# Kernel tuning notes

Hardware: AMD Instinct MI355X
Metric: run time of the kernel (lower is better)

Reference implementation:

```python
import jax, jax.numpy as jnp
import numpy as np

B, S, D, H, K, MLP, ZD = 8, 2048, 1024, 16, 256, 4096, 1024
DH = D // H
EPS = 1e-6


def setup_inputs() -> dict:
    key = jax.random.key(0)
    ks = jax.random.split(key, 32)
    g = lambda i, shape, scale=0.02: jax.random.normal(ks[i], shape, dtype=jnp.float32) * scale
    inp = {
        "x": jax.random.normal(ks[0], (B, S, D), dtype=jnp.float32),
        "z": jax.random.normal(ks[1], (B, ZD), dtype=jnp.float32),
        # attention projections
        "wq": g(2, (D, D)), "bq": jnp.zeros((D,), jnp.float32),
        "wk": g(3, (D, D)), "bk": jnp.zeros((D,), jnp.float32),
        "wv": g(4, (D, D)), "bv": jnp.zeros((D,), jnp.float32),
        # Linformer sequence projections (kernel over seq dim)
        "Ew": g(5, (S, K)), "Eb": jnp.zeros((K,), jnp.float32),
        "Fw": g(6, (S, K)), "Fb": jnp.zeros((K,), jnp.float32),
        "wo": g(7, (D, D)), "bo": jnp.zeros((D,), jnp.float32),
        # adaLN 1
        "h1w": g(8, (ZD, D)), "h1b": jnp.zeros((D,), jnp.float32),
        "g1w": g(9, (D, D)), "g1b": jnp.ones((D,), jnp.float32),
        "be1w": g(10, (D, D)), "be1b": jnp.zeros((D,), jnp.float32),
        # adaLN 2
        "h2w": g(11, (ZD, D)), "h2b": jnp.zeros((D,), jnp.float32),
        "g2w": g(12, (D, D)), "g2b": jnp.ones((D,), jnp.float32),
        "be2w": g(13, (D, D)), "be2b": jnp.zeros((D,), jnp.float32),
        # MLP
        "m1w": g(14, (D, MLP)), "m1b": jnp.zeros((MLP,), jnp.float32),
        "m2w": g(15, (MLP, D)), "m2b": jnp.zeros((D,), jnp.float32),
    }
    return inp


def _adaln(x, z, hw, hb, gw, gb, bw, bb):
    # moments over feature axis, normalize, then conditioned scale/shift
    mean = jnp.mean(x, axis=2, keepdims=True)
    var = jnp.var(x, axis=2, keepdims=True)
    xn = (x - mean) * jax.lax.rsqrt(var + EPS)
    h = jax.nn.silu(z @ hw + hb)              # [B, D]
    scale = h @ gw + gb                        # [B, D]
    offset = h @ bw + bb                       # [B, D]
    return xn * scale[:, None, :] + offset[:, None, :]


def _linformer_attn(x, wq, bq, wk, bk, wv, bv, Ew, Eb, Fw, Fb, wo, bo):
    q = (x @ wq + bq).reshape(B, S, H, DH).transpose(0, 2, 1, 3)  # [B,H,S,dh]
    k = (x @ wk + bk).reshape(B, S, H, DH).transpose(0, 2, 1, 3)
    v = (x @ wv + bv).reshape(B, S, H, DH).transpose(0, 2, 1, 3)
    # project seq dim S -> K (Dense applied to [B,H,dh,S]); bias adds on K axis
    k = jnp.einsum('bhsd,sk->bhkd', k, Ew) + Eb[None, None, :, None]  # [B,H,K,dh]
    v = jnp.einsum('bhsd,sk->bhkd', v, Fw) + Fb[None, None, :, None]
    scores = jnp.einsum('bhsd,bhkd->bhsk', q, k) / jnp.sqrt(jnp.float32(DH))
    attn = jax.nn.softmax(scores, axis=-1)
    out = jnp.einsum('bhsk,bhkd->bhsd', attn, v)  # [B,H,S,dh]
    out = out.transpose(0, 2, 1, 3).reshape(B, S, D)
    return out @ wo + bo


def reference(x, z, wq, bq, wk, bk, wv, bv, Ew, Eb, Fw, Fb, wo, bo,
              h1w, h1b, g1w, g1b, be1w, be1b,
              h2w, h2b, g2w, g2b, be2w, be2b,
              m1w, m1b, m2w, m2b):
    x1 = _adaln(x, z, h1w, h1b, g1w, g1b, be1w, be1b)
    attn_out = x + _linformer_attn(x1, wq, bq, wk, bk, wv, bv, Ew, Eb, Fw, Fb, wo, bo)
    x2 = _adaln(attn_out, z, h2w, h2b, g2w, g2b, be2w, be2b)
    hmid = jax.nn.gelu(x2 @ m1w + m1b, approximate=False)
    mlp_out = hmid @ m2w + m2b
    return mlp_out + attn_out
```

## Files before the change

### kernel.cpp

```cpp
#include <hip/hip_runtime.h>
#include <math.h>

#define AS1 __attribute__((address_space(1)))
#define AS3 __attribute__((address_space(3)))

typedef short bf16x8 __attribute__((ext_vector_type(8)));
typedef short s16x4  __attribute__((ext_vector_type(4)));
typedef float f32x4  __attribute__((ext_vector_type(4)));

#define MFMA(a,b,c) __builtin_amdgcn_mfma_f32_16x16x32_bf16((a),(b),(c),0,0,0)

__device__ __forceinline__ short f2bf(float f) {
  union { float f; unsigned u; } v; v.f = f;
  unsigned r = v.u + 0x7FFFu + ((v.u >> 16) & 1u);
  return (short)(r >> 16);
}

__device__ __forceinline__ void gload16(const void* g, void* l) {
  __builtin_amdgcn_global_load_lds((const AS1 void*)g, (AS3 void*)l, 16, 0, 0);
}

__global__ __launch_bounds__(256) void k_transpose_cvt(
    const float* __restrict__ in, short* __restrict__ out, int R, int C) {
  __shared__ float t[64][65];
  int c0 = blockIdx.x * 64, r0 = blockIdx.y * 64;
  int tx = threadIdx.x & 63, ty = threadIdx.x >> 6;
  for (int r = ty; r < 64; r += 4)
    t[r][tx] = in[(size_t)(r0 + r) * C + c0 + tx];
  __syncthreads();
  for (int c = ty; c < 64; c += 4)
    out[(size_t)(c0 + c) * R + r0 + tx] = f2bf(t[tx][c]);
}

__global__ __launch_bounds__(256) void k_cond_h(
    const float* __restrict__ z,
    const float* __restrict__ h1w, const float* __restrict__ h1b,
    const float* __restrict__ h2w, const float* __restrict__ h2b,
    float* __restrict__ hbuf) {
  int dl = threadIdx.x & 63, kq = threadIdx.x >> 6;
  int d = blockIdx.x * 64 + dl;
  int b = blockIdx.y, sel = blockIdx.z;
  const float* W = (sel ? h2w : h1w) + (size_t)(kq * 256) * 1024 + d;
  const float* zr = z + b * 1024 + kq * 256;
  float acc = 0.f;
  for (int i = 0; i < 256; ++i) acc = fmaf(zr[i], W[(size_t)i * 1024], acc);
  __shared__ float red[256];
  red[threadIdx.x] = acc;
  __syncthreads();
  if (kq == 0) {
    float v = red[dl] + red[dl + 64] + red[dl + 128] + red[dl + 192];
    v += (sel ? h2b : h1b)[d];
    hbuf[(size_t)(sel * 8 + b) * 1024 + d] = v / (1.f + expf(-v));
  }
}

__global__ __launch_bounds__(256) void k_cond_so(
    const float* __restrict__ hbuf,
    const float* __restrict__ g1w, const float* __restrict__ g1b,
    const float* __restrict__ be1w, const float* __restrict__ be1b,
    const float* __restrict__ g2w, const float* __restrict__ g2b,
    const float* __restrict__ be2w, const float* __restrict__ be2b,
    float* __restrict__ so) {
  int dl = threadIdx.x & 63, kq = threadIdx.x >> 6;
  int d = blockIdx.x * 64 + dl;
  int b = blockIdx.y, sel = blockIdx.z;
  const float* W = sel == 0 ? g1w : sel == 1 ? be1w : sel == 2 ? g2w : be2w;
  const float* bias = sel == 0 ? g1b : sel == 1 ? be1b : sel == 2 ? g2b : be2b;
  const float* hr = hbuf + (size_t)((sel >> 1) * 8 + b) * 1024 + kq * 256;
  const float* Wp = W + (size_t)(kq * 256) * 1024 + d;
  float acc = 0.f;
  for (int i = 0; i < 256; ++i) acc = fmaf(hr[i], Wp[(size_t)i * 1024], acc);
  __shared__ float red[256];
  red[threadIdx.x] = acc;
  __syncthreads();
  if (kq == 0) {
    float v = red[dl] + red[dl + 64] + red[dl + 128] + red[dl + 192] + bias[d];
    so[(size_t)(sel * 8 + b) * 1024 + d] = v;
  }
}

__global__ __launch_bounds__(256) void k_adaln(
    const float* __restrict__ xin, const float* __restrict__ so,
    int which, short* __restrict__ xout) {
  int row = blockIdx.x;
  int b = row >> 11;
  const float4* xr = (const float4*)(xin + (size_t)row * 1024);
  float4 v = xr[threadIdx.x];
  float s = v.x + v.y + v.z + v.w;
  float sq = v.x * v.x + v.y * v.y + v.z * v.z + v.w * v.w;
#pragma unroll
  for (int o = 32; o >= 1; o >>= 1) {
    s += __shfl_xor(s, o, 64);
    sq += __shfl_xor(sq, o, 64);
  }
  __shared__ float red[8];
  int wid = threadIdx.x >> 6;
  if ((threadIdx.x & 63) == 0) { red[wid] = s; red[4 + wid] = sq; }
  __syncthreads();
  s = red[0] + red[1] + red[2] + red[3];
  sq = red[4] + red[5] + red[6] + red[7];
  float mean = s * (1.f / 1024.f);
  float var = sq * (1.f / 1024.f) - mean * mean;
  float rstd = rsqrtf(var + 1e-6f);
  const float4* scp = (const float4*)(so + (size_t)(which * 2) * 8192 + b * 1024);
  const float4* ofp = (const float4*)(so + (size_t)(which * 2 + 1) * 8192 + b * 1024);
  float4 sc = scp[threadIdx.x], of = ofp[threadIdx.x];
  s16x4 o;
  o[0] = f2bf((v.x - mean) * rstd * sc.x + of.x);
  o[1] = f2bf((v.y - mean) * rstd * sc.y + of.y);
  o[2] = f2bf((v.z - mean) * rstd * sc.z + of.z);
  o[3] = f2bf((v.w - mean) * rstd * sc.w + of.w);
  *(s16x4*)(xout + (size_t)row * 1024 + threadIdx.x * 4) = o;
}

enum { EPI_QKV = 0, EPI_KP = 1, EPI_VPT = 2, EPI_RESID = 3, EPI_GELU = 4 };

template <int EPI>
__global__ __launch_bounds__(256) void k_gemm(
    const short* __restrict__ A, long sA, int lda,
    const short* __restrict__ BT, long sBT, int ldbt,
    int Kd,
    short* __restrict__ o0, short* __restrict__ o1, short* __restrict__ o2,
    const float* __restrict__ b0, const float* __restrict__ b1,
    const float* __restrict__ b2,
    const float* __restrict__ resid, float* __restrict__ fo, long sC) {
  int t = threadIdx.x, lane = t & 63, wid = t >> 6;
  int wr = wid >> 1, wc = wid & 1;
  int n0 = blockIdx.x * 128, m0 = blockIdx.y * 128, bz = blockIdx.z;
  const short* Ab = A + (long)bz * sA;
  const short* Bb = BT + (long)bz * sBT;
  __shared__ short lds[8192];
  const short* gA = Ab + (long)(m0 + (t >> 2)) * lda + (t & 3) * 8;
  const short* gB = Bb + (long)(n0 + (t >> 2)) * ldbt + (t & 3) * 8;
  char* lA = (char*)lds + wid * 1024;
  char* lB = (char*)lds + 8192 + wid * 1024;
  const long a64 = (long)64 * lda, b64s = (long)64 * ldbt;
  f32x4 acc[4][4];
#pragma unroll
  for (int m = 0; m < 4; ++m)
#pragma unroll
    for (int n = 0; n < 4; ++n) acc[m][n] = (f32x4){0.f, 0.f, 0.f, 0.f};

  int rsel = lane & 15, koff = (lane >> 4) * 16;
  for (int k = 0; k < Kd; k += 32) {
    gload16(gA, lA);
    gload16(gA + a64, lA + 4096);
    gload16(gB, lB);
    gload16(gB + b64s, lB + 4096);
    gA += 32; gB += 32;
    __syncthreads();
    bf16x8 af[4], bfr[4];
#pragma unroll
    for (int m = 0; m < 4; ++m)
      af[m] = *(const bf16x8*)((const char*)lds + (wr * 64 + m * 16 + rsel) * 64 + koff);
#pragma unroll
    for (int n = 0; n < 4; ++n)
      bfr[n] = *(const bf16x8*)((const char*)lds + 8192 + (wc * 64 + n * 16 + rsel) * 64 + koff);
#pragma unroll
    for (int m = 0; m < 4; ++m)
#pragma unroll
      for (int n = 0; n < 4; ++n)
        acc[m][n] = MFMA(af[m], bfr[n], acc[m][n]);
    __syncthreads();
  }

  int cl = lane & 15, rh = lane >> 4;
#pragma unroll
  for (int m = 0; m < 4; ++m) {
    int rgb = m0 + wr * 64 + m * 16 + rh * 4;
#pragma unroll
    for (int n = 0; n < 4; ++n) {
      int cg = n0 + wc * 64 + n * 16 + cl;
      f32x4 a = acc[m][n];
      if constexpr (EPI == EPI_QKV) {
        int sec = n0 >> 10;
        int cloc = cg & 1023;
        float bias = (sec == 0 ? b0 : sec == 1 ? b1 : b2)[cloc];
        if (sec == 0) {
#pragma unroll
          for (int r = 0; r < 4; ++r)
            o0[(size_t)(rgb + r) * 1024 + cloc] = f2bf(a[r] + bias);
        } else {
          short* dst = (sec == 1) ? o1 : o2;
          int bb = rgb >> 11, sl = rgb & 2047;
          s16x4 pk;
#pragma unroll
          for (int r = 0; r < 4; ++r) pk[r] = f2bf(a[r] + bias);
          *(s16x4*)(dst + ((long)bb * 1024 + cloc) * 2048 + sl) = pk;
        }
      } else if constexpr (EPI == EPI_KP) {
        short* dst = o0 + (long)bz * sC;
#pragma unroll
        for (int r = 0; r < 4; ++r)
          dst[(size_t)(rgb + r) * 1024 + cg] = f2bf(a[r] + b0[rgb + r]);
      } else if constexpr (EPI == EPI_VPT) {
        short* dst = o0 + (long)bz * sC;
        s16x4 pk;
#pragma unroll
        for (int r = 0; r < 4; ++r) pk[r] = f2bf(a[r] + b0[rgb + r]);
        *(s16x4*)(dst + (long)cg * 256 + rgb) = pk;
      } else if constexpr (EPI == EPI_RESID) {
        float bias = b0[cg];
#pragma unroll
        for (int r = 0; r < 4; ++r) {
          size_t idx = (size_t)(rgb + r) * 1024 + cg;
          fo[idx] = a[r] + bias + resid[idx];
        }
      } else if constexpr (EPI == EPI_GELU) {
        float bias = b0[cg];
#pragma unroll
        for (int r = 0; r < 4; ++r) {
          float xv = a[r] + bias;
          float g = 0.5f * xv * (1.f + erff(xv * 0.70710678118654752f));
          o0[(size_t)(rgb + r) * 4096 + cg] = f2bf(g);
        }
      }
    }
  }
}

__global__ __launch_bounds__(256) void k_attn(
    const short* __restrict__ q, const short* __restrict__ kp,
    const short* __restrict__ vpt, short* __restrict__ oh) {
  int lane = threadIdx.x & 63, wid = threadIdx.x >> 6;
  int h = blockIdx.y, b = blockIdx.z;
  int s0 = blockIdx.x * 64 + wid * 16;
  int cl = lane & 15, rh = lane >> 4;
  __shared__ short plds[4][16][264];

  const short* qbase = q + ((size_t)(b * 2048 + s0 + cl)) * 1024 + h * 64 + rh * 8;
  bf16x8 qa0 = *(const bf16x8*)qbase;
  bf16x8 qa1 = *(const bf16x8*)(qbase + 32);

  f32x4 sc[16];
  const short* kb = kp + ((size_t)(b * 256 + cl)) * 1024 + h * 64 + rh * 8;
#pragma unroll
  for (int n = 0; n < 16; ++n) {
    const short* kn = kb + (size_t)(n * 16) * 1024;
    f32x4 a = (f32x4){0.f, 0.f, 0.f, 0.f};
    a = MFMA(qa0, *(const bf16x8*)kn, a);
    a = MFMA(qa1, *(const bf16x8*)(kn + 32), a);
    sc[n] = a * 0.125f;
  }

  float mx[4] = {-1e30f, -1e30f, -1e30f, -1e30f};
#pragma unroll
  for (int n = 0; n < 16; ++n)
#pragma unroll
    for (int r = 0; r < 4; ++r) mx[r] = fmaxf(mx[r], sc[n][r]);
#pragma unroll
  for (int o = 1; o < 16; o <<= 1)
#pragma unroll
    for (int r = 0; r < 4; ++r) mx[r] = fmaxf(mx[r], __shfl_xor(mx[r], o, 64));

  float sm[4] = {0.f, 0.f, 0.f, 0.f};
#pragma unroll
  for (int n = 0; n < 16; ++n)
#pragma unroll
    for (int r = 0; r < 4; ++r) {
      float e = expf(sc[n][r] - mx[r]);
      sc[n][r] = e;
      sm[r] += e;
    }
#pragma unroll
  for (int o = 1; o < 16; o <<= 1)
#pragma unroll
    for (int r = 0; r < 4; ++r) sm[r] += __shfl_xor(sm[r], o, 64);
  float inv[4];
#pragma unroll
  for (int r = 0; r < 4; ++r) inv[r] = 1.f / sm[r];

#pragma unroll
  for (int n = 0; n < 16; ++n)
#pragma unroll
    for (int r = 0; r < 4; ++r)
      plds[wid][rh * 4 + r][n * 16 + cl] = f2bf(sc[n][r] * inv[r]);
  asm volatile("s_waitcnt lgkmcnt(0)" ::: "memory");

  bf16x8 pa[8];
#pragma unroll
  for (int c = 0; c < 8; ++c)
    pa[c] = *(const bf16x8*)&plds[wid][cl][c * 32 + rh * 8];

  const short* vb = vpt + ((size_t)(b * 1024 + h * 64 + cl)) * 256 + rh * 8;
  short* ob = oh + ((size_t)(b * 2048 + s0 + rh * 4)) * 1024 + h * 64 + cl;
#pragma unroll
  for (int n = 0; n < 4; ++n) {
    f32x4 a = (f32x4){0.f, 0.f, 0.f, 0.f};
    const short* vn = vb + (size_t)(n * 16) * 256;
#pragma unroll
    for (int c = 0; c < 8; ++c)
      a = MFMA(pa[c], *(const bf16x8*)(vn + c * 32), a);
#pragma unroll
    for (int r = 0; r < 4; ++r)
      ob[(size_t)r * 1024 + n * 16] = f2bf(a[r]);
  }
}

extern "C" void kernel_launch(void* const* d_in, const int* in_sizes, int n_in,
                              void* d_out, int out_size, void* d_ws, size_t ws_size,
                              hipStream_t stream) {
  (void)in_sizes; (void)n_in; (void)out_size; (void)ws_size;
  const float* x    = (const float*)d_in[0];
  const float* z    = (const float*)d_in[1];
  const float* wq   = (const float*)d_in[2];
  const float* bq   = (const float*)d_in[3];
  const float* wk   = (const float*)d_in[4];
  const float* bk   = (const float*)d_in[5];
  const float* wv   = (const float*)d_in[6];
  const float* bv   = (const float*)d_in[7];
  const float* Ew   = (const float*)d_in[8];
  const float* Eb   = (const float*)d_in[9];
  const float* Fw   = (const float*)d_in[10];
  const float* Fb   = (const float*)d_in[11];
  const float* wo   = (const float*)d_in[12];
  const float* bo   = (const float*)d_in[13];
  const float* h1w  = (const float*)d_in[14];
  const float* h1b  = (const float*)d_in[15];
  const float* g1w  = (const float*)d_in[16];
  const float* g1b  = (const float*)d_in[17];
  const float* be1w = (const float*)d_in[18];
  const float* be1b = (const float*)d_in[19];
  const float* h2w  = (const float*)d_in[20];
  const float* h2b  = (const float*)d_in[21];
  const float* g2w  = (const float*)d_in[22];
  const float* g2b  = (const float*)d_in[23];
  const float* be2w = (const float*)d_in[24];
  const float* be2b = (const float*)d_in[25];
  const float* m1w  = (const float*)d_in[26];
  const float* m1b  = (const float*)d_in[27];
  const float* m2w  = (const float*)d_in[28];
  const float* m2b  = (const float*)d_in[29];
  float* out = (float*)d_out;

  char* ws = (char*)d_ws;
  size_t off = 0;
  auto alloc = [&](size_t bytes) {
    char* p = ws + off;
    off += (bytes + 255) & ~(size_t)255;
    return p;
  };
  short* x1  = (short*)alloc((size_t)32 << 20);
  short* qb  = (short*)alloc((size_t)32 << 20);
  short* kT  = (short*)alloc((size_t)32 << 20);
  short* vT  = (short*)alloc((size_t)32 << 20);
  short* ah  = (short*)alloc((size_t)32 << 20);
  short* kpj = (short*)alloc((size_t)4 << 20);
  short* vpt = (short*)alloc((size_t)4 << 20);
  short* wqkvT = (short*)alloc((size_t)3072 * 1024 * 2);
  short* woT   = (short*)alloc((size_t)1024 * 1024 * 2);
  short* m1T   = (short*)alloc((size_t)4096 * 1024 * 2);
  short* m2T   = (short*)alloc((size_t)1024 * 4096 * 2);
  short* EwT   = (short*)alloc((size_t)256 * 2048 * 2);
  short* FwT   = (short*)alloc((size_t)256 * 2048 * 2);
  float* hbuf  = (float*)alloc((size_t)2 * 8 * 1024 * 4);
  float* sobuf = (float*)alloc((size_t)4 * 8 * 1024 * 4);
  float* aout = (float*)kT;
  short* x2   = ah;
  short* hmid = x1;

  dim3 blk(256);
  k_transpose_cvt<<<dim3(16, 16), blk, 0, stream>>>(wq, wqkvT, 1024, 1024);
  k_transpose_cvt<<<dim3(16, 16), blk, 0, stream>>>(wk, wqkvT + 1024 * 1024, 1024, 1024);
  k_transpose_cvt<<<dim3(16, 16), blk, 0, stream>>>(wv, wqkvT + 2 * 1024 * 1024, 1024, 1024);
  k_transpose_cvt<<<dim3(16, 16), blk, 0, stream>>>(wo, woT, 1024, 1024);
  k_transpose_cvt<<<dim3(64, 16), blk, 0, stream>>>(m1w, m1T, 1024, 4096);
  k_transpose_cvt<<<dim3(16, 64), blk, 0, stream>>>(m2w, m2T, 4096, 1024);
  k_transpose_cvt<<<dim3(4, 32), blk, 0, stream>>>(Ew, EwT, 2048, 256);
  k_transpose_cvt<<<dim3(4, 32), blk, 0, stream>>>(Fw, FwT, 2048, 256);
  k_cond_h<<<dim3(16, 8, 2), blk, 0, stream>>>(z, h1w, h1b, h2w, h2b, hbuf);
  k_cond_so<<<dim3(16, 8, 4), blk, 0, stream>>>(hbuf, g1w, g1b, be1w, be1b,
                                                g2w, g2b, be2w, be2b, sobuf);
  k_adaln<<<dim3(16384), blk, 0, stream>>>(x, sobuf, 0, x1);
  k_gemm<EPI_QKV><<<dim3(24, 128, 1), blk, 0, stream>>>(
      x1, 0, 1024, wqkvT, 0, 1024, 1024,
      qb, kT, vT, bq, bk, bv, nullptr, nullptr, 0);
  k_gemm<EPI_KP><<<dim3(8, 2, 8), blk, 0, stream>>>(
      EwT, 0, 2048, kT, (long)1024 * 2048, 2048, 2048,
      kpj, nullptr, nullptr, Eb, nullptr, nullptr, nullptr, nullptr, 262144);
  k_gemm<EPI_VPT><<<dim3(8, 2, 8), blk, 0, stream>>>(
      FwT, 0, 2048, vT, (long)1024 * 2048, 2048, 2048,
      vpt, nullptr, nullptr, Fb, nullptr, nullptr, nullptr, nullptr, 262144);
  k_attn<<<dim3(32, 16, 8), blk, 0, stream>>>(qb, kpj, vpt, ah);
  k_gemm<EPI_RESID><<<dim3(8, 128, 1), blk, 0, stream>>>(
      ah, 0, 1024, woT, 0, 1024, 1024,
      nullptr, nullptr, nullptr, bo, nullptr, nullptr, x, aout, 0);
  k_adaln<<<dim3(16384), blk, 0, stream>>>(aout, sobuf, 1, x2);
  for (int c = 0; c < 2; ++c) {
    const short* x2c = x2 + (size_t)c * 8192 * 1024;
    const float* aoc = aout + (size_t)c * 8192 * 1024;
    float* outc = out + (size_t)c * 8192 * 1024;
    k_gemm<EPI_GELU><<<dim3(32, 64, 1), blk, 0, stream>>>(
        x2c, 0, 1024, m1T, 0, 1024, 1024,
        hmid, nullptr, nullptr, m1b, nullptr, nullptr, nullptr, nullptr, 0);
    k_gemm<EPI_RESID><<<dim3(8, 64, 1), blk, 0, stream>>>(
        hmid, 0, 4096, m2T, 0, 4096, 4096,
        nullptr, nullptr, nullptr, m2b, nullptr, nullptr, aoc, outc, 0);
  }
}
```

Before: 1.065 ms.

## Add 256x256-tile 8-wave GEMM with double-buffered LDS pipeline for dense projections

Adds a new GEMM kernel with 256x256 output tiles, 512 threads and a 128 KB double-buffered LDS ring. Global-to-LDS loads are interleaved with phased MFMA blocks, using XOR-swizzled LDS addressing, s_setprio and a grid swizzle for L2 locality. The QKV, output-projection and both MLP GEMMs move to this kernel, while the small Linformer projections keep the old 128-tile kernel. The aim is more data reuse per tile and better overlap of loads with MFMA. The cost is higher register and LDS pressure, and fewer workgroups for the smaller GEMMs (128 and 256 blocks), which may underfill the GPU.

After: 1.116 ms. +4.8%, slower.

```diff
diff --git a/kernel.cpp b/kernel.cpp
--- a/kernel.cpp
+++ b/kernel.cpp
@@ -172,23 +172,7 @@
     for (int n = 0; n < 4; ++n) {
       int cg = n0 + wc * 64 + n * 16 + cl;
       f32x4 a = acc[m][n];
-      if constexpr (EPI == EPI_QKV) {
-        int sec = n0 >> 10;
-        int cloc = cg & 1023;
-        float bias = (sec == 0 ? b0 : sec == 1 ? b1 : b2)[cloc];
-        if (sec == 0) {
-#pragma unroll
-          for (int r = 0; r < 4; ++r)
-            o0[(size_t)(rgb + r) * 1024 + cloc] = f2bf(a[r] + bias);
-        } else {
-          short* dst = (sec == 1) ? o1 : o2;
-          int bb = rgb >> 11, sl = rgb & 2047;
-          s16x4 pk;
-#pragma unroll
-          for (int r = 0; r < 4; ++r) pk[r] = f2bf(a[r] + bias);
-          *(s16x4*)(dst + ((long)bb * 1024 + cloc) * 2048 + sl) = pk;
-        }
-      } else if constexpr (EPI == EPI_KP) {
+      if constexpr (EPI == EPI_KP) {
         short* dst = o0 + (long)bz * sC;
 #pragma unroll
         for (int r = 0; r < 4; ++r)
@@ -199,15 +183,155 @@
 #pragma unroll
         for (int r = 0; r < 4; ++r) pk[r] = f2bf(a[r] + b0[rgb + r]);
         *(s16x4*)(dst + (long)cg * 256 + rgb) = pk;
+      }
+    }
+  }
+}
+
+template <int EPI>
+__global__ __launch_bounds__(512, 2) void k_gemm256(
+    const short* __restrict__ A, int lda,
+    const short* __restrict__ BT, int ldbt,
+    int Kd, int ntN,
+    short* __restrict__ o0, short* __restrict__ o1, short* __restrict__ o2,
+    const float* __restrict__ bi0, const float* __restrict__ bi1,
+    const float* __restrict__ bi2,
+    const float* __restrict__ resid, float* __restrict__ fo) {
+  __shared__ __align__(16) char lds[131072];
+  int t = threadIdx.x, lane = t & 63, wid = t >> 6;
+  int wr = wid >> 2, wc = wid & 3;
+  int l15 = lane & 15;
+  int lko = ((lane >> 4) * 16) ^ (((l15 >> 2) & 1) << 5);
+
+  int nwg = gridDim.x, o = blockIdx.x;
+  int swz = (o & 7) * (nwg >> 3) + (o >> 3);
+  int mt = swz / ntN, nt = swz - mt * ntN;
+  int m0 = mt * 256, n0 = nt * 256;
+
+  int p0 = t * 16;
+  int sl = p0 ^ (((p0 >> 9) & 1) << 5);
+  int srow = sl >> 7, scol = sl & 127;
+  const char* A8 = (const char*)A;
+  const char* B8 = (const char*)BT;
+  size_t ldab = (size_t)lda * 2, ldbb = (size_t)ldbt * 2;
+  size_t aoff = (size_t)(m0 + srow) * ldab + scol;
+  size_t boff = (size_t)(n0 + srow) * ldbb + scol;
+  char* ldsw = (char*)lds + wid * 1024;
+
+  auto stage = [&](int H, int kt, int buf) {
+    char* d = ldsw + buf * 65536 + H * 16384;
+    if (H < 2) {
+      const char* s = A8 + aoff + (size_t)(H * 128) * ldab + (size_t)kt * 128;
+      gload16(s, d);
+      gload16(s + 64 * ldab, d + 8192);
+    } else {
+      const char* s = B8 + boff + (size_t)((H - 2) * 128) * ldbb + (size_t)kt * 128;
+      gload16(s, d);
+      gload16(s + 64 * ldbb, d + 8192);
+    }
+  };
+
+  const char* LA = (const char*)lds + wr * 16384 + l15 * 128 + lko;
+  const char* LB = (const char*)lds + 32768 + (wc >> 1) * 16384 + (wc & 1) * 8192 +
+                   l15 * 128 + lko;
+
+  f32x4 acc[8][4];
+#pragma unroll
+  for (int m = 0; m < 8; ++m)
+#pragma unroll
+    for (int n = 0; n < 4; ++n) acc[m][n] = (f32x4){0.f, 0.f, 0.f, 0.f};
+
+  bf16x8 af[4][2], Bv0[2][2], Bv1[2][2];
+
+#define RDA(buf, mi, ks) (*(const bf16x8*)(LA + (buf) * 65536 + (mi) * 2048 + (ks) * 64))
+#define RDB(buf, ni, ks) (*(const bf16x8*)(LB + (buf) * 65536 + (ni) * 2048 + (ks) * 64))
+#define PH_TAIL(MB, NB, BARR)                                         \
+  __builtin_amdgcn_s_barrier();                                       \
+  asm volatile("s_waitcnt lgkmcnt(0)" ::: "memory");                  \
+  __builtin_amdgcn_sched_barrier(0);                                  \
+  __builtin_amdgcn_s_setprio(1);                                      \
+  _Pragma("unroll") for (int mi = 0; mi < 4; ++mi)                    \
+  _Pragma("unroll") for (int ni = 0; ni < 2; ++ni)                    \
+  _Pragma("unroll") for (int ks = 0; ks < 2; ++ks)                    \
+      acc[(MB) + mi][(NB) + ni] =                                     \
+          MFMA(af[mi][ks], BARR[ni][ks], acc[(MB) + mi][(NB) + ni]);  \
+  __builtin_amdgcn_s_setprio(0);                                      \
+  __builtin_amdgcn_s_barrier();
+
+  int NT = Kd >> 6, NI = NT >> 1, msk = NT - 1;
+
+  stage(0, 0, 0); stage(1, 0, 0); stage(2, 0, 0); stage(3, 0, 0);
+  stage(0, 1, 1);
+  asm volatile("s_waitcnt vmcnt(2)" ::: "memory");
+  __builtin_amdgcn_s_barrier();
+
+  auto half = [&](int bf, int tkA, int bufA, int tkB, int bufB) {
+#pragma unroll
+    for (int mi = 0; mi < 4; ++mi)
+#pragma unroll
+      for (int ks = 0; ks < 2; ++ks) af[mi][ks] = RDA(bf, mi, ks);
+#pragma unroll
+    for (int ni = 0; ni < 2; ++ni)
+#pragma unroll
+      for (int ks = 0; ks < 2; ++ks) Bv0[ni][ks] = RDB(bf, ni, ks);
+    stage(1, tkA, bufA);
+    PH_TAIL(0, 0, Bv0)
+#pragma unroll
+    for (int ni = 0; ni < 2; ++ni)
+#pragma unroll
+      for (int ks = 0; ks < 2; ++ks) Bv1[ni][ks] = RDB(bf, ni + 2, ks);
+    stage(2, tkA, bufA);
+    PH_TAIL(0, 2, Bv1)
+#pragma unroll
+    for (int mi = 0; mi < 4; ++mi)
+#pragma unroll
+      for (int ks = 0; ks < 2; ++ks) af[mi][ks] = RDA(bf, mi + 4, ks);
+    stage(3, tkA, bufA);
+    PH_TAIL(4, 2, Bv1)
+    stage(0, tkB, bufB);
+    asm volatile("s_waitcnt vmcnt(2)" ::: "memory");
+    PH_TAIL(4, 0, Bv0)
+  };
+
+  for (int i = 0; i < NI; ++i) {
+    int T1k = 2 * i + 1, T2k = (2 * i + 2) & msk, T3k = (2 * i + 3) & msk;
+    half(0, T1k, 1, T2k, 0);
+    half(1, T2k, 0, T3k, 1);
+  }
+
+  int cl = l15, rh = lane >> 4;
+#pragma unroll
+  for (int m = 0; m < 8; ++m) {
+    int rgb = m0 + wr * 128 + m * 16 + rh * 4;
+#pragma unroll
+    for (int n = 0; n < 4; ++n) {
+      int cg = n0 + wc * 64 + n * 16 + cl;
+      f32x4 a = acc[m][n];
+      if constexpr (EPI == EPI_QKV) {
+        int sec = n0 >> 10;
+        int cloc = cg & 1023;
+        float bias = (sec == 0 ? bi0 : sec == 1 ? bi1 : bi2)[cloc];
+        if (sec == 0) {
+#pragma unroll
+          for (int r = 0; r < 4; ++r)
+            o0[(size_t)(rgb + r) * 1024 + cloc] = f2bf(a[r] + bias);
+        } else {
+          short* dst = (sec == 1) ? o1 : o2;
+          int bb = rgb >> 11, slc = rgb & 2047;
+          s16x4 pk;
+#pragma unroll
+          for (int r = 0; r < 4; ++r) pk[r] = f2bf(a[r] + bias);
+          *(s16x4*)(dst + ((long)bb * 1024 + cloc) * 2048 + slc) = pk;
+        }
       } else if constexpr (EPI == EPI_RESID) {
-        float bias = b0[cg];
+        float bias = bi0[cg];
 #pragma unroll
         for (int r = 0; r < 4; ++r) {
           size_t idx = (size_t)(rgb + r) * 1024 + cg;
           fo[idx] = a[r] + bias + resid[idx];
         }
       } else if constexpr (EPI == EPI_GELU) {
-        float bias = b0[cg];
+        float bias = bi0[cg];
 #pragma unroll
         for (int r = 0; r < 4; ++r) {
           float xv = a[r] + bias;
@@ -217,6 +341,9 @@
       }
     }
   }
+#undef RDA
+#undef RDB
+#undef PH_TAIL
 }
 
 __global__ __launch_bounds__(256) void k_attn(
@@ -372,9 +499,9 @@
   k_cond_so<<<dim3(16, 8, 4), blk, 0, stream>>>(hbuf, g1w, g1b, be1w, be1b,
                                                 g2w, g2b, be2w, be2b, sobuf);
   k_adaln<<<dim3(16384), blk, 0, stream>>>(x, sobuf, 0, x1);
-  k_gemm<EPI_QKV><<<dim3(24, 128, 1), blk, 0, stream>>>(
-      x1, 0, 1024, wqkvT, 0, 1024, 1024,
-      qb, kT, vT, bq, bk, bv, nullptr, nullptr, 0);
+  k_gemm256<EPI_QKV><<<dim3(768), dim3(512), 0, stream>>>(
+      x1, 1024, wqkvT, 1024, 1024, 12,
+      qb, kT, vT, bq, bk, bv, nullptr, nullptr);
   k_gemm<EPI_KP><<<dim3(8, 2, 8), blk, 0, stream>>>(
       EwT, 0, 2048, kT, (long)1024 * 2048, 2048, 2048,
       kpj, nullptr, nullptr, Eb, nullptr, nullptr, nullptr, nullptr, 262144);
@@ -382,19 +509,19 @@
       FwT, 0, 2048, vT, (long)1024 * 2048, 2048, 2048,
       vpt, nullptr, nullptr, Fb, nullptr, nullptr, nullptr, nullptr, 262144);
   k_attn<<<dim3(32, 16, 8), blk, 0, stream>>>(qb, kpj, vpt, ah);
-  k_gemm<EPI_RESID><<<dim3(8, 128, 1), blk, 0, stream>>>(
-      ah, 0, 1024, woT, 0, 1024, 1024,
-      nullptr, nullptr, nullptr, bo, nullptr, nullptr, x, aout, 0);
+  k_gemm256<EPI_RESID><<<dim3(256), dim3(512), 0, stream>>>(
+      ah, 1024, woT, 1024, 1024, 4,
+      nullptr, nullptr, nullptr, bo, nullptr, nullptr, x, aout);
   k_adaln<<<dim3(16384), blk, 0, stream>>>(aout, sobuf, 1, x2);
   for (int c = 0; c < 2; ++c) {
     const short* x2c = x2 + (size_t)c * 8192 * 1024;
     const float* aoc = aout + (size_t)c * 8192 * 1024;
     float* outc = out + (size_t)c * 8192 * 1024;
-    k_gemm<EPI_GELU><<<dim3(32, 64, 1), blk, 0, stream>>>(
-        x2c, 0, 1024, m1T, 0, 1024, 1024,
-        hmid, nullptr, nullptr, m1b, nullptr, nullptr, nullptr, nullptr, 0);
-    k_gemm<EPI_RESID><<<dim3(8, 64, 1), blk, 0, stream>>>(
-        hmid, 0, 4096, m2T, 0, 4096, 4096,
-        nullptr, nullptr, nullptr, m2b, nullptr, nullptr, aoc, outc, 0);
-  }
-}
+    k_gemm256<EPI_GELU><<<dim3(512), dim3(512), 0, stream>>>(
+        x2c, 1024, m1T, 1024, 1024, 16,
+        hmid, nullptr, nullptr, m1b, nullptr, nullptr, nullptr, nullptr);
+    k_gemm256<EPI_RESID><<<dim3(128), dim3(512), 0, stream>>>(
+        hmid, 4096, m2T, 4096, 4096, 4,
+        nullptr, nullptr, nullptr, m2b, nullptr, nullptr, aoc, outc);
+  }
+}
```

## Merge K/V Linformer projections into one launch and add 256x256 GEMM for MLP1

Applied to the files above, without the earlier changes.

Combines the separate K and V sequence-projection GEMMs into a single launch, using the z grid dimension to select which one a block computes. Adds a new 512-thread GEMM kernel with 256x256 tiles, double-buffered LDS with swizzled layout, grid swizzle and MFMA priority bumps, and uses it for the first MLP up-projection chunk. The aim is to cut launch overhead and improve data reuse and latency hiding in the largest GEMM. In exchange it uses 128KB of LDS per block, which limits occupancy, and the second chunk still runs on the old kernel.

After: 1.167 ms. 1.1x slower.

```diff
diff --git a/kernel.cpp b/kernel.cpp
--- a/kernel.cpp
+++ b/kernel.cpp
@@ -113,7 +113,7 @@
   *(s16x4*)(xout + (size_t)row * 1024 + threadIdx.x * 4) = o;
 }
 
-enum { EPI_QKV = 0, EPI_KP = 1, EPI_VPT = 2, EPI_RESID = 3, EPI_GELU = 4 };
+enum { EPI_QKV = 0, EPI_KVP = 1, EPI_RESID = 3, EPI_GELU = 4 };
 
 template <int EPI>
 __global__ __launch_bounds__(256) void k_gemm(
@@ -127,8 +127,17 @@
   int t = threadIdx.x, lane = t & 63, wid = t >> 6;
   int wr = wid >> 1, wc = wid & 1;
   int n0 = blockIdx.x * 128, m0 = blockIdx.y * 128, bz = blockIdx.z;
-  const short* Ab = A + (long)bz * sA;
-  const short* Bb = BT + (long)bz * sBT;
+  int batch = bz, sel = 0;
+  if constexpr (EPI == EPI_KVP) { batch = bz & 7; sel = bz >> 3; }
+  const short* Ab;
+  const short* Bb;
+  if constexpr (EPI == EPI_KVP) {
+    Ab = sel ? (const short*)o2 : A;
+    Bb = BT + (long)sel * 16777216 + (long)batch * sBT;
+  } else {
+    Ab = A + (long)batch * sA;
+    Bb = BT + (long)batch * sBT;
+  }
   __shared__ short lds[8192];
   const short* gA = Ab + (long)(m0 + (t >> 2)) * lda + (t & 3) * 8;
   const short* gB = Bb + (long)(n0 + (t >> 2)) * ldbt + (t & 3) * 8;
@@ -188,17 +197,19 @@
           for (int r = 0; r < 4; ++r) pk[r] = f2bf(a[r] + bias);
           *(s16x4*)(dst + ((long)bb * 1024 + cloc) * 2048 + sl) = pk;
         }
-      } else if constexpr (EPI == EPI_KP) {
-        short* dst = o0 + (long)bz * sC;
-#pragma unroll
-        for (int r = 0; r < 4; ++r)
-          dst[(size_t)(rgb + r) * 1024 + cg] = f2bf(a[r] + b0[rgb + r]);
-      } else if constexpr (EPI == EPI_VPT) {
-        short* dst = o0 + (long)bz * sC;
-        s16x4 pk;
-#pragma unroll
-        for (int r = 0; r < 4; ++r) pk[r] = f2bf(a[r] + b0[rgb + r]);
-        *(s16x4*)(dst + (long)cg * 256 + rgb) = pk;
+      } else if constexpr (EPI == EPI_KVP) {
+        const float* bias = sel ? b1 : b0;
+        short* dst = (sel ? o1 : o0) + (long)batch * sC;
+        if (sel == 0) {
+#pragma unroll
+          for (int r = 0; r < 4; ++r)
+            dst[(size_t)(rgb + r) * 1024 + cg] = f2bf(a[r] + bias[rgb + r]);
+        } else {
+          s16x4 pk;
+#pragma unroll
+          for (int r = 0; r < 4; ++r) pk[r] = f2bf(a[r] + bias[rgb + r]);
+          *(s16x4*)(dst + (long)cg * 256 + rgb) = pk;
+        }
       } else if constexpr (EPI == EPI_RESID) {
         float bias = b0[cg];
 #pragma unroll
@@ -213,6 +224,119 @@
           float xv = a[r] + bias;
           float g = 0.5f * xv * (1.f + erff(xv * 0.70710678118654752f));
           o0[(size_t)(rgb + r) * 4096 + cg] = f2bf(g);
+        }
+      }
+    }
+  }
+}
+
+template <int EPI>
+__global__ __launch_bounds__(512, 2) void k_gemm256p2(
+    const short* __restrict__ A, int lda,
+    const short* __restrict__ BT, int ldbt,
+    int Kd, int ntN,
+    short* __restrict__ o0, const float* __restrict__ bi0,
+    const float* __restrict__ resid, float* __restrict__ fo) {
+  __shared__ __align__(16) char lds[131072];
+  int t = threadIdx.x, lane = t & 63, wid = t >> 6;
+  int wr = wid >> 2, wc = wid & 3;
+  int l15 = lane & 15;
+  int q16x = ((lane >> 4) * 16) ^ ((l15 & 3) << 4);
+  int kf64 = ((l15 >> 2) & 1) << 6;
+  int k0o = kf64, k1o = 64 - kf64;
+
+  int nwg = gridDim.x, o = blockIdx.x;
+  int swz = (o & 7) * (nwg >> 3) + (o >> 3);
+  int mt = swz / ntN, nt = swz - mt * ntN;
+  int m0 = mt * 256, n0 = nt * 256;
+
+  int p0 = t * 16;
+  int srow = p0 >> 7;
+  int scol = (p0 & 127) ^ ((srow & 7) << 4);
+  size_t ldab = (size_t)lda * 2, ldbb = (size_t)ldbt * 2;
+  const char* sA0 = (const char*)A + (size_t)(m0 + srow) * ldab + scol;
+  const char* sA1 = sA0 + 128 * ldab;
+  const char* sB0 = (const char*)BT + (size_t)(n0 + srow) * ldbb + scol;
+  const char* sB1 = sB0 + 128 * ldbb;
+  char* ldsw = (char*)lds + wid * 1024;
+  size_t a64 = ldab << 6, b64 = ldbb << 6;
+
+  auto stage = [&](int kt, int buf) {
+    char* d = ldsw + buf * 65536;
+    size_t ko = (size_t)kt << 7;
+    gload16(sA0 + ko, d);           gload16(sA0 + ko + a64, d + 8192);
+    gload16(sA1 + ko, d + 16384);   gload16(sA1 + ko + a64, d + 24576);
+    gload16(sB0 + ko, d + 32768);   gload16(sB0 + ko + b64, d + 40960);
+    gload16(sB1 + ko, d + 49152);   gload16(sB1 + ko + b64, d + 57344);
+  };
+
+  const char* LAb = (const char*)lds + wr * 16384 + l15 * 128 + q16x;
+  const char* LBb = (const char*)lds + 32768 + (wc >> 1) * 16384 + (wc & 1) * 8192 +
+                    l15 * 128 + q16x;
+
+  f32x4 acc[8][4];
+#pragma unroll
+  for (int m = 0; m < 8; ++m)
+#pragma unroll
+    for (int n = 0; n < 4; ++n) acc[m][n] = (f32x4){0.f, 0.f, 0.f, 0.f};
+
+  int NT = Kd >> 6;
+  stage(0, 0);
+  asm volatile("s_waitcnt vmcnt(0)" ::: "memory");
+  __builtin_amdgcn_s_barrier();
+
+  for (int tt = 0; tt < NT; ++tt) {
+    int cur = tt & 1;
+    int nxt = (tt + 1 < NT) ? tt + 1 : 0;
+    stage(nxt, cur ^ 1);
+    const char* LA = LAb + cur * 65536;
+    const char* LB = LBb + cur * 65536;
+    bf16x8 af[8][2], bfr[4][2];
+#pragma unroll
+    for (int mi = 0; mi < 8; ++mi)
+#pragma unroll
+      for (int ks = 0; ks < 2; ++ks)
+        af[mi][ks] = *(const bf16x8*)(LA + mi * 2048 + (ks ? k1o : k0o));
+#pragma unroll
+    for (int ni = 0; ni < 4; ++ni)
+#pragma unroll
+      for (int ks = 0; ks < 2; ++ks)
+        bfr[ni][ks] = *(const bf16x8*)(LB + ni * 2048 + (ks ? k1o : k0o));
+    __builtin_amdgcn_s_setprio(1);
+#pragma unroll
+    for (int mi = 0; mi < 8; ++mi)
+#pragma unroll
+      for (int ni = 0; ni < 4; ++ni)
+#pragma unroll
+        for (int ks = 0; ks < 2; ++ks)
+          acc[mi][ni] = MFMA(af[mi][ks], bfr[ni][ks], acc[mi][ni]);
+    __builtin_amdgcn_s_setprio(0);
+    asm volatile("s_waitcnt vmcnt(0)" ::: "memory");
+    __builtin_amdgcn_s_barrier();
+  }
+
+  int cl = l15, rh = lane >> 4;
+#pragma unroll
+  for (int m = 0; m < 8; ++m) {
+    int rgb = m0 + wr * 128 + m * 16 + rh * 4;
+#pragma unroll
+    for (int n = 0; n < 4; ++n) {
+      int cg = n0 + wc * 64 + n * 16 + cl;
+      f32x4 a = acc[m][n];
+      if constexpr (EPI == EPI_GELU) {
+        float bias = bi0[cg];
+#pragma unroll
+        for (int r = 0; r < 4; ++r) {
+          float xv = a[r] + bias;
+          float g = 0.5f * xv * (1.f + erff(xv * 0.70710678118654752f));
+          o0[(size_t)(rgb + r) * 4096 + cg] = f2bf(g);
+        }
+      } else if constexpr (EPI == EPI_RESID) {
+        float bias = bi0[cg];
+#pragma unroll
+        for (int r = 0; r < 4; ++r) {
+          size_t idx = (size_t)(rgb + r) * 1024 + cg;
+          fo[idx] = a[r] + bias + resid[idx];
         }
       }
     }
@@ -375,21 +499,23 @@
   k_gemm<EPI_QKV><<<dim3(24, 128, 1), blk, 0, stream>>>(
       x1, 0, 1024, wqkvT, 0, 1024, 1024,
       qb, kT, vT, bq, bk, bv, nullptr, nullptr, 0);
-  k_gemm<EPI_KP><<<dim3(8, 2, 8), blk, 0, stream>>>(
+  k_gemm<EPI_KVP><<<dim3(8, 2, 16), blk, 0, stream>>>(
       EwT, 0, 2048, kT, (long)1024 * 2048, 2048, 2048,
-      kpj, nullptr, nullptr, Eb, nullptr, nullptr, nullptr, nullptr, 262144);
-  k_gemm<EPI_VPT><<<dim3(8, 2, 8), blk, 0, stream>>>(
-      FwT, 0, 2048, vT, (long)1024 * 2048, 2048, 2048,
-      vpt, nullptr, nullptr, Fb, nullptr, nullptr, nullptr, nullptr, 262144);
+      kpj, vpt, FwT, Eb, Fb, nullptr, nullptr, nullptr, 262144);
   k_attn<<<dim3(32, 16, 8), blk, 0, stream>>>(qb, kpj, vpt, ah);
   k_gemm<EPI_RESID><<<dim3(8, 128, 1), blk, 0, stream>>>(
       ah, 0, 1024, woT, 0, 1024, 1024,
       nullptr, nullptr, nullptr, bo, nullptr, nullptr, x, aout, 0);
   k_adaln<<<dim3(16384), blk, 0, stream>>>(aout, sobuf, 1, x2);
-  for (int c = 0; c < 2; ++c) {
-    const short* x2c = x2 + (size_t)c * 8192 * 1024;
-    const float* aoc = aout + (size_t)c * 8192 * 1024;
-    float* outc = out + (size_t)c * 8192 * 1024;
+  k_gemm256p2<EPI_GELU><<<dim3(512), dim3(512), 0, stream>>>(
+      x2, 1024, m1T, 1024, 1024, 16, hmid, m1b, nullptr, nullptr);
+  k_gemm<EPI_RESID><<<dim3(8, 64, 1), blk, 0, stream>>>(
+      hmid, 0, 4096, m2T, 0, 4096, 4096,
+      nullptr, nullptr, nullptr, m2b, nullptr, nullptr, aout, out, 0);
+  {
+    const short* x2c = x2 + (size_t)8192 * 1024;
+    const float* aoc = aout + (size_t)8192 * 1024;
+    float* outc = out + (size_t)8192 * 1024;
     k_gemm<EPI_GELU><<<dim3(32, 64, 1), blk, 0, stream>>>(
         x2c, 0, 1024, m1T, 0, 1024, 1024,
         hmid, nullptr, nullptr, m1b, nullptr, nullptr, nullptr, nullptr, 0);
```

## Reassociate Linformer K/V projections to project x over sequence first

Applied to the files above, without the earlier changes.

Instead of computing full K and V projections over all 2048 positions and then projecting the sequence down to 256, the code first projects the normalized input x1 along the sequence with E and F (via a bf16 transpose of x1). It then applies wk/wv to the reduced 256-row tensors, folding the biases in through column sums of E and F. This removes two large S×D×D GEMMs and their transposed writes, at the cost of an extra transpose pass over x1. The four square weight transposes are also merged into one launch, and the first MLP up-projection chunk uses a new 64-wide-K swizzled GEMM kernel.

Measured after the change: 1.107 ms. +3.9%, slower.

```diff
diff --git a/kernel.cpp b/kernel.cpp
--- a/kernel.cpp
+++ b/kernel.cpp
@@ -30,6 +30,48 @@
   __syncthreads();
   for (int c = ty; c < 64; c += 4)
     out[(size_t)(c0 + c) * R + r0 + tx] = f2bf(t[tx][c]);
+}
+
+__global__ __launch_bounds__(256) void k_transpose_cvt4(
+    const float* __restrict__ s0, const float* __restrict__ s1,
+    const float* __restrict__ s2, const float* __restrict__ s3,
+    short* __restrict__ d0, short* __restrict__ d1,
+    short* __restrict__ d2, short* __restrict__ d3) {
+  int zz = blockIdx.z;
+  const float* in = zz == 0 ? s0 : zz == 1 ? s1 : zz == 2 ? s2 : s3;
+  short* out = zz == 0 ? d0 : zz == 1 ? d1 : zz == 2 ? d2 : d3;
+  __shared__ float t[64][65];
+  int c0 = blockIdx.x * 64, r0 = blockIdx.y * 64;
+  int tx = threadIdx.x & 63, ty = threadIdx.x >> 6;
+  for (int r = ty; r < 64; r += 4)
+    t[r][tx] = in[(size_t)(r0 + r) * 1024 + c0 + tx];
+  __syncthreads();
+  for (int c = ty; c < 64; c += 4)
+    out[(size_t)(c0 + c) * 1024 + r0 + tx] = f2bf(t[tx][c]);
+}
+
+__global__ __launch_bounds__(256) void k_transpose_bf16(
+    const short* __restrict__ in, short* __restrict__ out) {
+  __shared__ short t[64][65];
+  int d0 = blockIdx.x * 64, s0 = blockIdx.y * 64, b = blockIdx.z;
+  int tx = threadIdx.x & 63, ty = threadIdx.x >> 6;
+  const short* src = in + ((size_t)(b * 2048 + s0)) * 1024 + d0;
+  for (int r = ty; r < 64; r += 4)
+    t[r][tx] = src[(size_t)r * 1024 + tx];
+  __syncthreads();
+  short* dst = out + ((size_t)(b * 1024 + d0)) * 2048 + s0;
+  for (int c = ty; c < 64; c += 4)
+    dst[(size_t)c * 2048 + tx] = t[tx][c];
+}
+
+__global__ __launch_bounds__(256) void k_colsum(
+    const float* __restrict__ Ew, const float* __restrict__ Fw,
+    float* __restrict__ cs) {
+  int ki = threadIdx.x, sel = blockIdx.x;
+  const float* W = sel ? Fw : Ew;
+  float s = 0.f;
+  for (int i = 0; i < 2048; ++i) s += W[(size_t)i * 256 + ki];
+  cs[sel * 256 + ki] = s;
 }
 
 __global__ __launch_bounds__(256) void k_cond_h(
@@ -113,7 +155,7 @@
   *(s16x4*)(xout + (size_t)row * 1024 + threadIdx.x * 4) = o;
 }
 
-enum { EPI_QKV = 0, EPI_KP = 1, EPI_VPT = 2, EPI_RESID = 3, EPI_GELU = 4 };
+enum { EPI_Q = 0, EPI_EF = 1, EPI_RESID = 3, EPI_GELU = 4 };
 
 template <int EPI>
 __global__ __launch_bounds__(256) void k_gemm(
@@ -121,14 +163,22 @@
     const short* __restrict__ BT, long sBT, int ldbt,
     int Kd,
     short* __restrict__ o0, short* __restrict__ o1, short* __restrict__ o2,
-    const float* __restrict__ b0, const float* __restrict__ b1,
-    const float* __restrict__ b2,
+    const float* __restrict__ b0,
     const float* __restrict__ resid, float* __restrict__ fo, long sC) {
   int t = threadIdx.x, lane = t & 63, wid = t >> 6;
   int wr = wid >> 1, wc = wid & 1;
   int n0 = blockIdx.x * 128, m0 = blockIdx.y * 128, bz = blockIdx.z;
-  const short* Ab = A + (long)bz * sA;
-  const short* Bb = BT + (long)bz * sBT;
+  int batch = bz, sel = 0;
+  if constexpr (EPI == EPI_EF) { batch = bz & 7; sel = bz >> 3; }
+  const short* Ab;
+  const short* Bb;
+  if constexpr (EPI == EPI_EF) {
+    Ab = sel ? (const short*)o2 : A;
+    Bb = BT + (long)batch * sBT;
+  } else {
+    Ab = A + (long)batch * sA;
+    Bb = BT + (long)batch * sBT;
+  }
   __shared__ short lds[8192];
   const short* gA = Ab + (long)(m0 + (t >> 2)) * lda + (t & 3) * 8;
   const short* gB = Bb + (long)(n0 + (t >> 2)) * ldbt + (t & 3) * 8;
@@ -172,33 +222,16 @@
     for (int n = 0; n < 4; ++n) {
       int cg = n0 + wc * 64 + n * 16 + cl;
       f32x4 a = acc[m][n];
-      if constexpr (EPI == EPI_QKV) {
-        int sec = n0 >> 10;
-        int cloc = cg & 1023;
-        float bias = (sec == 0 ? b0 : sec == 1 ? b1 : b2)[cloc];
-        if (sec == 0) {
-#pragma unroll
-          for (int r = 0; r < 4; ++r)
-            o0[(size_t)(rgb + r) * 1024 + cloc] = f2bf(a[r] + bias);
-        } else {
-          short* dst = (sec == 1) ? o1 : o2;
-          int bb = rgb >> 11, sl = rgb & 2047;
-          s16x4 pk;
-#pragma unroll
-          for (int r = 0; r < 4; ++r) pk[r] = f2bf(a[r] + bias);
-          *(s16x4*)(dst + ((long)bb * 1024 + cloc) * 2048 + sl) = pk;
-        }
-      } else if constexpr (EPI == EPI_KP) {
-        short* dst = o0 + (long)bz * sC;
+      if constexpr (EPI == EPI_Q) {
+        float bias = b0[cg];
 #pragma unroll
         for (int r = 0; r < 4; ++r)
-          dst[(size_t)(rgb + r) * 1024 + cg] = f2bf(a[r] + b0[rgb + r]);
-      } else if constexpr (EPI == EPI_VPT) {
-        short* dst = o0 + (long)bz * sC;
-        s16x4 pk;
-#pragma unroll
-        for (int r = 0; r < 4; ++r) pk[r] = f2bf(a[r] + b0[rgb + r]);
-        *(s16x4*)(dst + (long)cg * 256 + rgb) = pk;
+          o0[(size_t)(rgb + r) * 1024 + cg] = f2bf(a[r] + bias);
+      } else if constexpr (EPI == EPI_EF) {
+        short* dst = (sel ? o1 : o0) + (long)batch * sC;
+#pragma unroll
+        for (int r = 0; r < 4; ++r)
+          dst[(size_t)(rgb + r) * 1024 + cg] = f2bf(a[r]);
       } else if constexpr (EPI == EPI_RESID) {
         float bias = b0[cg];
 #pragma unroll
@@ -214,6 +247,154 @@
           float g = 0.5f * xv * (1.f + erff(xv * 0.70710678118654752f));
           o0[(size_t)(rgb + r) * 4096 + cg] = f2bf(g);
         }
+      }
+    }
+  }
+}
+
+__global__ __launch_bounds__(256) void k_kvproj(
+    const short* __restrict__ xe, const short* __restrict__ xf,
+    const short* __restrict__ wkT, const short* __restrict__ wvT,
+    const float* __restrict__ Eb, const float* __restrict__ Fb,
+    const float* __restrict__ bk, const float* __restrict__ bv,
+    const float* __restrict__ cs,
+    short* __restrict__ kpj, short* __restrict__ vpt) {
+  int t = threadIdx.x, lane = t & 63, wid = t >> 6;
+  int wr = wid >> 1, wc = wid & 1;
+  int n0 = blockIdx.x * 128, m0 = blockIdx.y * 128, bz = blockIdx.z;
+  int batch = bz & 7, sel = bz >> 3;
+  const short* Ab = (sel ? xf : xe) + (long)batch * 262144;
+  const short* Bb = sel ? wvT : wkT;
+  __shared__ short lds[8192];
+  const short* gA = Ab + (long)(m0 + (t >> 2)) * 1024 + (t & 3) * 8;
+  const short* gB = Bb + (long)(n0 + (t >> 2)) * 1024 + (t & 3) * 8;
+  char* lA = (char*)lds + wid * 1024;
+  char* lB = (char*)lds + 8192 + wid * 1024;
+  const long a64 = (long)64 * 1024;
+  f32x4 acc[4][4];
+#pragma unroll
+  for (int m = 0; m < 4; ++m)
+#pragma unroll
+    for (int n = 0; n < 4; ++n) acc[m][n] = (f32x4){0.f, 0.f, 0.f, 0.f};
+
+  int rsel = lane & 15, koff = (lane >> 4) * 16;
+  for (int k = 0; k < 1024; k += 32) {
+    gload16(gA, lA);
+    gload16(gA + a64, lA + 4096);
+    gload16(gB, lB);
+    gload16(gB + a64, lB + 4096);
+    gA += 32; gB += 32;
+    __syncthreads();
+    bf16x8 af[4], bfr[4];
+#pragma unroll
+    for (int m = 0; m < 4; ++m)
+      af[m] = *(const bf16x8*)((const char*)lds + (wr * 64 + m * 16 + rsel) * 64 + koff);
+#pragma unroll
+    for (int n = 0; n < 4; ++n)
+      bfr[n] = *(const bf16x8*)((const char*)lds + 8192 + (wc * 64 + n * 16 + rsel) * 64 + koff);
+#pragma unroll
+    for (int m = 0; m < 4; ++m)
+#pragma unroll
+      for (int n = 0; n < 4; ++n)
+        acc[m][n] = MFMA(af[m], bfr[n], acc[m][n]);
+    __syncthreads();
+  }
+
+  const float* rb = sel ? Fb : Eb;
+  const float* cb = sel ? bv : bk;
+  int cl = lane & 15, rh = lane >> 4;
+#pragma unroll
+  for (int m = 0; m < 4; ++m) {
+    int rgb = m0 + wr * 64 + m * 16 + rh * 4;
+#pragma unroll
+    for (int n = 0; n < 4; ++n) {
+      int cg = n0 + wc * 64 + n * 16 + cl;
+      f32x4 a = acc[m][n];
+      float bc = cb[cg];
+      if (sel == 0) {
+#pragma unroll
+        for (int r = 0; r < 4; ++r)
+          kpj[((long)batch * 256 + rgb + r) * 1024 + cg] =
+              f2bf(a[r] + rb[rgb + r] + cs[rgb + r] * bc);
+      } else {
+        s16x4 pk;
+#pragma unroll
+        for (int r = 0; r < 4; ++r)
+          pk[r] = f2bf(a[r] + rb[rgb + r] + cs[256 + rgb + r] * bc);
+        *(s16x4*)(vpt + ((long)batch * 1024 + cg) * 256 + rgb) = pk;
+      }
+    }
+  }
+}
+
+__global__ __launch_bounds__(256) void k_gemm64gelu(
+    const short* __restrict__ A, int lda,
+    const short* __restrict__ BT, int ldbt, int Kd,
+    short* __restrict__ o0, const float* __restrict__ b0) {
+  __shared__ __align__(16) char lds[32768];
+  int t = threadIdx.x, lane = t & 63, wid = t >> 6;
+  int wr = wid >> 1, wc = wid & 1, l15 = lane & 15;
+  int q16x = ((lane >> 4) * 16) ^ ((l15 & 3) << 4);
+  int k0o = ((l15 >> 2) & 1) << 6, k1o = 64 - k0o;
+  int n0 = blockIdx.x * 128, m0 = blockIdx.y * 128;
+  int p0 = t * 16;
+  int srow = p0 >> 7, scol = (p0 & 127) ^ ((srow & 7) << 4);
+  size_t ldab = (size_t)lda * 2, ldbb = (size_t)ldbt * 2;
+  const char* gA = (const char*)A + (size_t)(m0 + srow) * ldab + scol;
+  const char* gB = (const char*)BT + (size_t)(n0 + srow) * ldbb + scol;
+  char* lw = (char*)lds + wid * 1024;
+  const char* LA = (const char*)lds + (wr * 64 + l15) * 128 + q16x;
+  const char* LB = (const char*)lds + 16384 + (wc * 64 + l15) * 128 + q16x;
+  f32x4 acc[4][4];
+#pragma unroll
+  for (int m = 0; m < 4; ++m)
+#pragma unroll
+    for (int n = 0; n < 4; ++n) acc[m][n] = (f32x4){0.f, 0.f, 0.f, 0.f};
+
+  for (int k = 0; k < Kd; k += 64) {
+    size_t ko = (size_t)k * 2;
+#pragma unroll
+    for (int g = 0; g < 4; ++g)
+      gload16(gA + (size_t)(g * 32) * ldab + ko, lw + g * 4096);
+#pragma unroll
+    for (int g = 0; g < 4; ++g)
+      gload16(gB + (size_t)(g * 32) * ldbb + ko, lw + 16384 + g * 4096);
+    __syncthreads();
+    bf16x8 af[4][2], bfr[4][2];
+#pragma unroll
+    for (int m = 0; m < 4; ++m)
+#pragma unroll
+      for (int ks = 0; ks < 2; ++ks)
+        af[m][ks] = *(const bf16x8*)(LA + m * 2048 + (ks ? k1o : k0o));
+#pragma unroll
+    for (int n = 0; n < 4; ++n)
+#pragma unroll
+      for (int ks = 0; ks < 2; ++ks)
+        bfr[n][ks] = *(const bf16x8*)(LB + n * 2048 + (ks ? k1o : k0o));
+#pragma unroll
+    for (int ks = 0; ks < 2; ++ks)
+#pragma unroll
+      for (int m = 0; m < 4; ++m)
+#pragma unroll
+        for (int n = 0; n < 4; ++n)
+          acc[m][n] = MFMA(af[m][ks], bfr[n][ks], acc[m][n]);
+    __syncthreads();
+  }
+
+  int cl = l15, rh = lane >> 4;
+#pragma unroll
+  for (int m = 0; m < 4; ++m) {
+    int rgb = m0 + wr * 64 + m * 16 + rh * 4;
+#pragma unroll
+    for (int n = 0; n < 4; ++n) {
+      int cg = n0 + wc * 64 + n * 16 + cl;
+      f32x4 a = acc[m][n];
+      float bias = b0[cg];
+#pragma unroll
+      for (int r = 0; r < 4; ++r) {
+        float xv = a[r] + bias;
+        float g = 0.5f * xv * (1.f + erff(xv * 0.70710678118654752f));
+        o0[(size_t)(rgb + r) * 4096 + cg] = f2bf(g);
       }
     }
   }
@@ -341,10 +522,12 @@
     return p;
   };
   short* x1  = (short*)alloc((size_t)32 << 20);
+  short* x1T = (short*)alloc((size_t)32 << 20);
+  short* hx  = (short*)alloc((size_t)32 << 20);
   short* qb  = (short*)alloc((size_t)32 << 20);
-  short* kT  = (short*)alloc((size_t)32 << 20);
-  short* vT  = (short*)alloc((size_t)32 << 20);
   short* ah  = (short*)alloc((size_t)32 << 20);
+  short* xe  = (short*)alloc((size_t)4 << 20);
+  short* xf  = (short*)alloc((size_t)4 << 20);
   short* kpj = (short*)alloc((size_t)4 << 20);
   short* vpt = (short*)alloc((size_t)4 << 20);
   short* wqkvT = (short*)alloc((size_t)3072 * 1024 * 2);
@@ -353,48 +536,54 @@
   short* m2T   = (short*)alloc((size_t)1024 * 4096 * 2);
   short* EwT   = (short*)alloc((size_t)256 * 2048 * 2);
   short* FwT   = (short*)alloc((size_t)256 * 2048 * 2);
+  float* csEF  = (float*)alloc(512 * 4);
   float* hbuf  = (float*)alloc((size_t)2 * 8 * 1024 * 4);
   float* sobuf = (float*)alloc((size_t)4 * 8 * 1024 * 4);
-  float* aout = (float*)kT;
+  float* aout = (float*)x1;
   short* x2   = ah;
-  short* hmid = x1;
+  short* hmid = hx;
+  short* wqT = wqkvT, *wkT = wqkvT + 1024 * 1024, *wvT = wqkvT + 2 * 1024 * 1024;
 
   dim3 blk(256);
-  k_transpose_cvt<<<dim3(16, 16), blk, 0, stream>>>(wq, wqkvT, 1024, 1024);
-  k_transpose_cvt<<<dim3(16, 16), blk, 0, stream>>>(wk, wqkvT + 1024 * 1024, 1024, 1024);
-  k_transpose_cvt<<<dim3(16, 16), blk, 0, stream>>>(wv, wqkvT + 2 * 1024 * 1024, 1024, 1024);
-  k_transpose_cvt<<<dim3(16, 16), blk, 0, stream>>>(wo, woT, 1024, 1024);
+  k_transpose_cvt4<<<dim3(16, 16, 4), blk, 0, stream>>>(wq, wk, wv, wo,
+                                                        wqT, wkT, wvT, woT);
   k_transpose_cvt<<<dim3(64, 16), blk, 0, stream>>>(m1w, m1T, 1024, 4096);
   k_transpose_cvt<<<dim3(16, 64), blk, 0, stream>>>(m2w, m2T, 4096, 1024);
   k_transpose_cvt<<<dim3(4, 32), blk, 0, stream>>>(Ew, EwT, 2048, 256);
   k_transpose_cvt<<<dim3(4, 32), blk, 0, stream>>>(Fw, FwT, 2048, 256);
+  k_colsum<<<dim3(2), blk, 0, stream>>>(Ew, Fw, csEF);
   k_cond_h<<<dim3(16, 8, 2), blk, 0, stream>>>(z, h1w, h1b, h2w, h2b, hbuf);
   k_cond_so<<<dim3(16, 8, 4), blk, 0, stream>>>(hbuf, g1w, g1b, be1w, be1b,
                                                 g2w, g2b, be2w, be2b, sobuf);
   k_adaln<<<dim3(16384), blk, 0, stream>>>(x, sobuf, 0, x1);
-  k_gemm<EPI_QKV><<<dim3(24, 128, 1), blk, 0, stream>>>(
-      x1, 0, 1024, wqkvT, 0, 1024, 1024,
-      qb, kT, vT, bq, bk, bv, nullptr, nullptr, 0);
-  k_gemm<EPI_KP><<<dim3(8, 2, 8), blk, 0, stream>>>(
-      EwT, 0, 2048, kT, (long)1024 * 2048, 2048, 2048,
-      kpj, nullptr, nullptr, Eb, nullptr, nullptr, nullptr, nullptr, 262144);
-  k_gemm<EPI_VPT><<<dim3(8, 2, 8), blk, 0, stream>>>(
-      FwT, 0, 2048, vT, (long)1024 * 2048, 2048, 2048,
-      vpt, nullptr, nullptr, Fb, nullptr, nullptr, nullptr, nullptr, 262144);
+  k_transpose_bf16<<<dim3(16, 32, 8), blk, 0, stream>>>(x1, x1T);
+  k_gemm<EPI_Q><<<dim3(8, 128, 1), blk, 0, stream>>>(
+      x1, 0, 1024, wqT, 0, 1024, 1024,
+      qb, nullptr, nullptr, bq, nullptr, nullptr, 0);
+  k_gemm<EPI_EF><<<dim3(8, 2, 16), blk, 0, stream>>>(
+      EwT, 0, 2048, x1T, (long)1024 * 2048, 2048, 2048,
+      xe, xf, (short*)FwT, nullptr, nullptr, nullptr, (long)256 * 1024);
+  k_kvproj<<<dim3(8, 2, 16), blk, 0, stream>>>(
+      xe, xf, wkT, wvT, Eb, Fb, bk, bv, csEF, kpj, vpt);
   k_attn<<<dim3(32, 16, 8), blk, 0, stream>>>(qb, kpj, vpt, ah);
   k_gemm<EPI_RESID><<<dim3(8, 128, 1), blk, 0, stream>>>(
       ah, 0, 1024, woT, 0, 1024, 1024,
-      nullptr, nullptr, nullptr, bo, nullptr, nullptr, x, aout, 0);
+      nullptr, nullptr, nullptr, bo, x, aout, 0);
   k_adaln<<<dim3(16384), blk, 0, stream>>>(aout, sobuf, 1, x2);
-  for (int c = 0; c < 2; ++c) {
-    const short* x2c = x2 + (size_t)c * 8192 * 1024;
-    const float* aoc = aout + (size_t)c * 8192 * 1024;
-    float* outc = out + (size_t)c * 8192 * 1024;
+  k_gemm64gelu<<<dim3(32, 64), blk, 0, stream>>>(
+      x2, 1024, m1T, 1024, 1024, hmid, m1b);
+  k_gemm<EPI_RESID><<<dim3(8, 64, 1), blk, 0, stream>>>(
+      hmid, 0, 4096, m2T, 0, 4096, 4096,
+      nullptr, nullptr, nullptr, m2b, aout, out, 0);
+  {
+    const short* x2c = x2 + (size_t)8192 * 1024;
+    const float* aoc = aout + (size_t)8192 * 1024;
+    float* outc = out + (size_t)8192 * 1024;
     k_gemm<EPI_GELU><<<dim3(32, 64, 1), blk, 0, stream>>>(
         x2c, 0, 1024, m1T, 0, 1024, 1024,
-        hmid, nullptr, nullptr, m1b, nullptr, nullptr, nullptr, nullptr, 0);
+        hmid, nullptr, nullptr, m1b, nullptr, nullptr, 0);
     k_gemm<EPI_RESID><<<dim3(8, 64, 1), blk, 0, stream>>>(
         hmid, 0, 4096, m2T, 0, 4096, 4096,
-        nullptr, nullptr, nullptr, m2b, nullptr, nullptr, aoc, outc, 0);
-  }
-}
+        nullptr, nullptr, nullptr, m2b, aoc, outc, 0);
+  }
+}
```
